# Kernel tuning notes

Measured on AMD Instinct MI355X. Metric: run time of the kernel, lower is better.

## Reference

```python
import jax, jax.numpy as jnp
import numpy as np

NUM_CLASSES = 20
STRIDE = 32
INPUT_SIZE = 2560
CONF_THRESH = 0.01
NMS_THRESH = 0.5
G = INPUT_SIZE // STRIDE          # 80 grid cells per side
N = G * G                         # 6400 candidate boxes
EPS = 1e-28                       # epsilon from original pure-python NMS


def _make_grid():
    # torch.meshgrid default 'ij' indexing: flat index n = x*G + y, entry [x, y]
    gx, gy = jnp.meshgrid(jnp.arange(G, dtype=jnp.float32),
                          jnp.arange(G, dtype=jnp.float32), indexing='ij')
    return jnp.stack([gx, gy], axis=-1).reshape(N, 2)


def _decode_boxes(txtytwth):
    # (grid + sigmoid(txty)) * stride -> center; exp(twth) -> width/height
    cxcy = (_make_grid() + jax.nn.sigmoid(txtytwth[:, :2])) * STRIDE
    wh = jnp.exp(txtytwth[:, 2:])
    boxes = jnp.concatenate([cxcy - wh * 0.5, cxcy + wh * 0.5], axis=-1)
    return jnp.clip(boxes / INPUT_SIZE, 0.0, 1.0)  # [N,4] xyxy in [0,1]


def _batched_nms(boxes, scores, class_idx):
    """Per-class greedy NMS via class-offset trick (equivalent to looping classes)."""
    # translate each class's boxes to a disjoint region so cross-class IoU ~ 0
    b = boxes + class_idx.astype(boxes.dtype)[:, None] * 2.0
    order = jnp.argsort(-scores)              # descending score order
    b = b[order]
    areas = (b[:, 2] - b[:, 0]) * (b[:, 3] - b[:, 1])
    xx1 = jnp.maximum(b[:, None, 0], b[None, :, 0])
    yy1 = jnp.maximum(b[:, None, 1], b[None, :, 1])
    xx2 = jnp.minimum(b[:, None, 2], b[None, :, 2])
    yy2 = jnp.minimum(b[:, None, 3], b[None, :, 3])
    w = jnp.maximum(EPS, xx2 - xx1)
    h = jnp.maximum(EPS, yy2 - yy1)
    inter = w * h                             # [N,N] pairwise intersection
    iou = inter / (areas[:, None] + areas[None, :] - inter)
    valid = scores[order] >= CONF_THRESH      # conf filter before NMS
    idxs = jnp.arange(N)

    def body(i, keep):
        supp = (iou[i] > NMS_THRESH) & (idxs > i)
        return jnp.where(keep[i], keep & ~supp, keep)

    keep_sorted = jax.lax.fori_loop(0, N, body, valid)
    return jnp.zeros(N, dtype=bool).at[order].set(keep_sorted)


def reference(pred):
    p = pred[0]                                   # inference path uses batch 0 only
    conf = jax.nn.sigmoid(p[:, :1])               # objectness
    cls_scores = jax.nn.softmax(p[:, 1:1 + NUM_CLASSES], axis=1) * conf
    boxes = _decode_boxes(p[:, 1 + NUM_CLASSES:])
    class_idx = jnp.argmax(cls_scores, axis=1)
    scores = jnp.max(cls_scores, axis=1)
    keep = _batched_nms(boxes, scores, class_idx)
    # fixed-shape outputs: non-kept detections have score zeroed, keep mask returned
    return boxes, scores * keep, class_idx.astype(jnp.int32), keep


def setup_inputs() -> dict:
    key = jax.random.key(0)
    pred = jax.random.normal(key, (1, N, 1 + NUM_CLASSES + 4), dtype=jnp.float32)
    return {"pred": pred}
```

## Files before the change

kernel.cpp:

```cpp
#include <hip/hip_runtime.h>
#include <stdint.h>

#define NBOX 6400
#define GRIDW 80
#define NC 20
#define NBLK 100

__device__ __forceinline__ float sigmoidf(float x) { return 1.0f / (1.0f + expf(-x)); }

__device__ __forceinline__ void decode_one(const float* __restrict__ p, int n,
        float4* box, float* score, int* cls) {
    float conf = sigmoidf(p[0]);
    float c[NC];
    float m = -INFINITY;
    #pragma unroll
    for (int j = 0; j < NC; j++) { c[j] = p[1 + j]; m = fmaxf(m, c[j]); }
    float sum = 0.f;
    #pragma unroll
    for (int j = 0; j < NC; j++) { c[j] = expf(c[j] - m); sum += c[j]; }
    float best = -INFINITY; int bi = 0;
    #pragma unroll
    for (int j = 0; j < NC; j++) {
        float s = (c[j] / sum) * conf;
        if (s > best) { best = s; bi = j; }
    }
    float gx = (float)(n / GRIDW);
    float gy = (float)(n % GRIDW);
    float cx = (gx + sigmoidf(p[21])) * 32.0f;
    float cy = (gy + sigmoidf(p[22])) * 32.0f;
    float w = expf(p[23]);
    float h = expf(p[24]);
    box->x = fminf(fmaxf((cx - w * 0.5f) / 2560.0f, 0.0f), 1.0f);
    box->y = fminf(fmaxf((cy - h * 0.5f) / 2560.0f, 0.0f), 1.0f);
    box->z = fminf(fmaxf((cx + w * 0.5f) / 2560.0f, 0.0f), 1.0f);
    box->w = fminf(fmaxf((cy + h * 0.5f) / 2560.0f, 0.0f), 1.0f);
    *score = best;
    *cls = bi;
}

__global__ __launch_bounds__(64) void k_decode(const float* __restrict__ pred,
        float* __restrict__ out, float4* __restrict__ boff,
        float* __restrict__ score_ws, float4* __restrict__ blkbb,
        uint64_t* __restrict__ validw) {
    int t = threadIdx.x;
    int n = blockIdx.x * 64 + t;
    float4 bx; float s; int cls;
    decode_one(pred + (size_t)n * 25, n, &bx, &s, &cls);
    ((float4*)out)[n] = bx;
    out[32000 + n] = (float)cls;
    bool valid = s >= 0.01f;
    out[25600 + n] = valid ? s : 0.0f;
    out[38400 + n] = valid ? 1.0f : 0.0f;
    score_ws[n] = s;
    float off = 2.0f * (float)cls;
    boff[n] = make_float4(bx.x + off, bx.y + off, bx.z + off, bx.w + off);

    float x1 = valid ? bx.x :  INFINITY;
    float y1 = valid ? bx.y :  INFINITY;
    float x2 = valid ? bx.z : -INFINITY;
    float y2 = valid ? bx.w : -INFINITY;
    #pragma unroll
    for (int d = 1; d < 64; d <<= 1) {
        x1 = fminf(x1, __shfl_xor(x1, d));
        y1 = fminf(y1, __shfl_xor(y1, d));
        x2 = fmaxf(x2, __shfl_xor(x2, d));
        y2 = fmaxf(y2, __shfl_xor(y2, d));
    }
    uint64_t vb = __ballot(valid);
    if (t == 0) {
        blkbb[blockIdx.x] = make_float4(x1, y1, x2, y2);
        validw[blockIdx.x] = vb;
    }
}

__global__ __launch_bounds__(64) void k_pairs(const float4* __restrict__ boff,
        const float4* __restrict__ blkbb, const uint64_t* __restrict__ validw,
        uint32_t* __restrict__ flag) {
    int k = blockIdx.x;
    float disc = (NBLK + 0.5f) * (NBLK + 0.5f) - 2.0f * (float)k;
    int bi = (int)((float)NBLK + 0.5f - sqrtf(disc));
    while (bi * NBLK - bi * (bi - 1) / 2 > k) bi--;
    while ((bi + 1) * NBLK - (bi + 1) * bi / 2 <= k) bi++;
    int bj = bi + (k - (bi * NBLK - bi * (bi - 1) / 2));

    float4 ra = blkbb[bi];
    float4 ca = blkbb[bj];
    const float M = 1e-5f;
    bool ov = (fminf(ra.z, ca.z) + M >= fmaxf(ra.x, ca.x)) &&
              (fminf(ra.w, ca.w) + M >= fmaxf(ra.y, ca.y));
    if (!ov) return;

    int t = threadIdx.x;
    __shared__ float4 cb[64];
    cb[t] = boff[bj * 64 + t];
    __syncthreads();
    uint64_t colvalid = validw[bj];
    uint64_t rowvalid = validw[bi];
    int i = bi * 64 + t;
    float4 rb = boff[i];
    float areai = (rb.z - rb.x) * (rb.w - rb.y);
    bool hit = false;
    if ((rowvalid >> t) & 1ull) {
        for (int s2 = 0; s2 < 64; s2++) {
            if (!((colvalid >> s2) & 1ull)) continue;
            int j = bj * 64 + s2;
            if (bi == bj && j <= i) continue;
            float4 b = cb[s2];
            float xx1 = fmaxf(rb.x, b.x);
            float yy1 = fmaxf(rb.y, b.y);
            float xx2 = fminf(rb.z, b.z);
            float yy2 = fminf(rb.w, b.w);
            float ww = fmaxf(1e-28f, xx2 - xx1);
            float hh = fmaxf(1e-28f, yy2 - yy1);
            float inter = ww * hh;
            float areaj = (b.z - b.x) * (b.w - b.y);
            if (3.0f * inter >= 0.9995f * (areai + areaj)) { hit = true; break; }
        }
    }
    if (__ballot(hit) != 0ull) {
        if (t == 0) flag[0] = 1u;
    }
}

__global__ __launch_bounds__(1024) void k_fixup(
        const uint32_t* __restrict__ flag, const float* __restrict__ score,
        const float4* __restrict__ boff, int* __restrict__ sidx,
        float* __restrict__ sscore, float4* __restrict__ sbox,
        float* __restrict__ out) {
    if (flag[0] != 1u) return;
    __shared__ uint64_t klds[NBOX];
    __shared__ uint32_t keepb[NBOX / 32];
    int t = threadIdx.x;
    for (int n = t; n < NBOX; n += 1024) {
        klds[n] = (((uint64_t)(~__float_as_uint(score[n]))) << 32) | (uint32_t)n;
    }
    __syncthreads();
    for (int n = t; n < NBOX; n += 1024) {
        uint64_t mk = klds[n];
        int r = 0;
        for (int j = 0; j < NBOX; j++) r += (klds[j] < mk) ? 1 : 0;
        sidx[r] = n;
        sscore[r] = score[n];
        sbox[r] = boff[n];
    }
    __syncthreads();
    for (int w2 = t; w2 < NBOX / 32; w2 += 1024) {
        uint32_t v = 0;
        for (int b = 0; b < 32; b++) v |= (sscore[w2 * 32 + b] >= 0.01f) ? (1u << b) : 0u;
        keepb[w2] = v;
    }
    __syncthreads();
    for (int i = 0; i < NBOX; i++) {
        bool kept = (keepb[i >> 5] >> (i & 31)) & 1u;
        if (kept) {
            float4 a = sbox[i];
            float areai = (a.z - a.x) * (a.w - a.y);
            for (int j = i + 1 + t; j < NBOX; j += 1024) {
                if ((keepb[j >> 5] >> (j & 31)) & 1u) {
                    float4 b = sbox[j];
                    float xx1 = fmaxf(a.x, b.x);
                    float yy1 = fmaxf(a.y, b.y);
                    float xx2 = fminf(a.z, b.z);
                    float yy2 = fminf(a.w, b.w);
                    float ww = fmaxf(1e-28f, xx2 - xx1);
                    float hh = fmaxf(1e-28f, yy2 - yy1);
                    float inter = ww * hh;
                    float areaj = (b.z - b.x) * (b.w - b.y);
                    float iou = inter / (areai + areaj - inter);
                    if (iou > 0.5f) atomicAnd(&keepb[j >> 5], ~(1u << (j & 31)));
                }
            }
        }
        __syncthreads();
    }
    for (int r = t; r < NBOX; r += 1024) {
        int orig = sidx[r];
        uint32_t kb = (keepb[r >> 5] >> (r & 31)) & 1u;
        out[38400 + orig] = (float)kb;
        out[25600 + orig] = kb ? sscore[r] : 0.0f;
    }
}

extern "C" void kernel_launch(void* const* d_in, const int* in_sizes, int n_in,
                              void* d_out, int out_size, void* d_ws, size_t ws_size,
                              hipStream_t stream) {
    const float* pred = (const float*)d_in[0];
    float* out = (float*)d_out;
    char* ws = (char*)d_ws;
    float4*   boff   = (float4*)(ws + 0);
    float*    score  = (float*)(ws + 102400);
    float4*   blkbb  = (float4*)(ws + 128000);
    uint64_t* validw = (uint64_t*)(ws + 129600);
    uint32_t* flag   = (uint32_t*)(ws + 130432);
    int*      sidx   = (int*)(ws + 131072);
    float*    sscore = (float*)(ws + 156672);
    float4*   sbox   = (float4*)(ws + 182272);

    k_decode<<<NBLK, 64, 0, stream>>>(pred, out, boff, score, blkbb, validw);
    k_pairs<<<5050, 64, 0, stream>>>(boff, blkbb, validw, flag);
    k_fixup<<<1, 1024, 0, stream>>>(flag, score, boff, sidx, sscore, sbox, out);
}
```

Baseline: 73.08 us.

## Merge pair check and fallback NMS into one kernel with last-block election

Replaces the 5050-block pair-check kernel and the separate single-block fixup kernel with one 25-block kernel. Each wave handles one row block and walks the overlapping column blocks found via ballot, reading column boxes through wave shuffles instead of LDS. A done counter picks the last block to run the exact NMS fallback when the flag is set. The flag and counter are now reset inside the decode kernel. This saves a kernel launch and the many short-lived blocks, at the cost of serial per-wave loops over column blocks and running any fallback on a 256-thread block instead of a 1024-thread one.

```diff
diff --git a/kernel.cpp b/kernel.cpp
--- a/kernel.cpp
+++ b/kernel.cpp
@@ -38,12 +38,15 @@
     *cls = bi;
 }
 
-__global__ __launch_bounds__(64) void k_decode(const float* __restrict__ pred,
+__global__ __launch_bounds__(256) void k_decode(const float* __restrict__ pred,
         float* __restrict__ out, float4* __restrict__ boff,
         float* __restrict__ score_ws, float4* __restrict__ blkbb,
-        uint64_t* __restrict__ validw) {
+        uint64_t* __restrict__ validw, uint32_t* __restrict__ flag,
+        uint32_t* __restrict__ done) {
     int t = threadIdx.x;
-    int n = blockIdx.x * 64 + t;
+    int n = blockIdx.x * 256 + t;
+    int l = t & 63;
+    if (n == 0) { flag[0] = 0u; done[0] = 0u; }
     float4 bx; float s; int cls;
     decode_one(pred + (size_t)n * 25, n, &bx, &s, &cls);
     ((float4*)out)[n] = bx;
@@ -67,75 +70,99 @@
         y2 = fmaxf(y2, __shfl_xor(y2, d));
     }
     uint64_t vb = __ballot(valid);
-    if (t == 0) {
-        blkbb[blockIdx.x] = make_float4(x1, y1, x2, y2);
-        validw[blockIdx.x] = vb;
-    }
-}
-
-__global__ __launch_bounds__(64) void k_pairs(const float4* __restrict__ boff,
+    if (l == 0) {
+        blkbb[n >> 6] = make_float4(x1, y1, x2, y2);
+        validw[n >> 6] = vb;
+    }
+}
+
+__global__ __launch_bounds__(256) void k_work(const float4* __restrict__ boff,
         const float4* __restrict__ blkbb, const uint64_t* __restrict__ validw,
-        uint32_t* __restrict__ flag) {
-    int k = blockIdx.x;
-    float disc = (NBLK + 0.5f) * (NBLK + 0.5f) - 2.0f * (float)k;
-    int bi = (int)((float)NBLK + 0.5f - sqrtf(disc));
-    while (bi * NBLK - bi * (bi - 1) / 2 > k) bi--;
-    while ((bi + 1) * NBLK - (bi + 1) * bi / 2 <= k) bi++;
-    int bj = bi + (k - (bi * NBLK - bi * (bi - 1) / 2));
+        const float* __restrict__ score, uint32_t* __restrict__ flag,
+        uint32_t* __restrict__ done, int* __restrict__ sidx,
+        float* __restrict__ sscore, float4* __restrict__ sbox,
+        float* __restrict__ out) {
+    __shared__ uint64_t klds[NBOX];
+    __shared__ uint32_t keepb[NBOX / 32];
+    __shared__ uint32_t lastf;
+    int t = threadIdx.x;
+    int w = t >> 6, l = t & 63;
+    int bi = blockIdx.x * 4 + w;
 
     float4 ra = blkbb[bi];
-    float4 ca = blkbb[bj];
+    uint64_t rowvalid = validw[bi];
     const float M = 1e-5f;
-    bool ov = (fminf(ra.z, ca.z) + M >= fmaxf(ra.x, ca.x)) &&
-              (fminf(ra.w, ca.w) + M >= fmaxf(ra.y, ca.y));
-    if (!ov) return;
-
-    int t = threadIdx.x;
-    __shared__ float4 cb[64];
-    cb[t] = boff[bj * 64 + t];
-    __syncthreads();
-    uint64_t colvalid = validw[bj];
-    uint64_t rowvalid = validw[bi];
-    int i = bi * 64 + t;
+    uint64_t surv_lo, surv_hi;
+    {
+        bool ov = false;
+        int bj = bi + l;
+        if (bj < NBLK) {
+            float4 ca = blkbb[bj];
+            ov = (fminf(ra.z, ca.z) + M >= fmaxf(ra.x, ca.x)) &&
+                 (fminf(ra.w, ca.w) + M >= fmaxf(ra.y, ca.y));
+        }
+        surv_lo = __ballot(ov);
+        ov = false;
+        bj = bi + 64 + l;
+        if (bj < NBLK) {
+            float4 ca = blkbb[bj];
+            ov = (fminf(ra.z, ca.z) + M >= fmaxf(ra.x, ca.x)) &&
+                 (fminf(ra.w, ca.w) + M >= fmaxf(ra.y, ca.y));
+        }
+        surv_hi = __ballot(ov);
+    }
+    if (rowvalid == 0ull) { surv_lo = 0ull; surv_hi = 0ull; }
+
+    int i = bi * 64 + l;
     float4 rb = boff[i];
     float areai = (rb.z - rb.x) * (rb.w - rb.y);
+    bool rv = (rowvalid >> l) & 1ull;
     bool hit = false;
-    if ((rowvalid >> t) & 1ull) {
-        for (int s2 = 0; s2 < 64; s2++) {
-            if (!((colvalid >> s2) & 1ull)) continue;
-            int j = bj * 64 + s2;
-            if (bi == bj && j <= i) continue;
-            float4 b = cb[s2];
-            float xx1 = fmaxf(rb.x, b.x);
-            float yy1 = fmaxf(rb.y, b.y);
-            float xx2 = fminf(rb.z, b.z);
-            float yy2 = fminf(rb.w, b.w);
-            float ww = fmaxf(1e-28f, xx2 - xx1);
-            float hh = fmaxf(1e-28f, yy2 - yy1);
-            float inter = ww * hh;
-            float areaj = (b.z - b.x) * (b.w - b.y);
-            if (3.0f * inter >= 0.9995f * (areai + areaj)) { hit = true; break; }
-        }
-    }
-    if (__ballot(hit) != 0ull) {
-        if (t == 0) flag[0] = 1u;
-    }
-}
-
-__global__ __launch_bounds__(1024) void k_fixup(
-        const uint32_t* __restrict__ flag, const float* __restrict__ score,
-        const float4* __restrict__ boff, int* __restrict__ sidx,
-        float* __restrict__ sscore, float4* __restrict__ sbox,
-        float* __restrict__ out) {
-    if (flag[0] != 1u) return;
-    __shared__ uint64_t klds[NBOX];
-    __shared__ uint32_t keepb[NBOX / 32];
-    int t = threadIdx.x;
-    for (int n = t; n < NBOX; n += 1024) {
+    while ((surv_lo | surv_hi) != 0ull) {
+        int d;
+        if (surv_lo) { d = __ffsll((unsigned long long)surv_lo) - 1; surv_lo &= surv_lo - 1; }
+        else { d = 64 + __ffsll((unsigned long long)surv_hi) - 1; surv_hi &= surv_hi - 1; }
+        int bj = bi + d;
+        uint64_t colvalid = validw[bj];
+        if (colvalid == 0ull) continue;
+        float4 cb = boff[bj * 64 + l];
+        if (rv && !hit) {
+            for (int s2 = 0; s2 < 64; s2++) {
+                if (!((colvalid >> s2) & 1ull)) continue;
+                int j = bj * 64 + s2;
+                if (bi == bj && j <= i) continue;
+                float bxx = __shfl(cb.x, s2);
+                float byy = __shfl(cb.y, s2);
+                float bzz = __shfl(cb.z, s2);
+                float bww = __shfl(cb.w, s2);
+                float xx1 = fmaxf(rb.x, bxx);
+                float yy1 = fmaxf(rb.y, byy);
+                float xx2 = fminf(rb.z, bzz);
+                float yy2 = fminf(rb.w, bww);
+                float ww = fmaxf(1e-28f, xx2 - xx1);
+                float hh = fmaxf(1e-28f, yy2 - yy1);
+                float inter = ww * hh;
+                float areaj = (bzz - bxx) * (bww - byy);
+                if (3.0f * inter >= 0.9995f * (areai + areaj)) { hit = true; break; }
+            }
+        }
+    }
+    if (__ballot(hit) != 0ull && l == 0) atomicOr(flag, 1u);
+
+    __syncthreads();
+    __threadfence();
+    if (t == 0) lastf = (atomicAdd(done, 1u) == 24u) ? 1u : 0u;
+    __syncthreads();
+    if (!lastf) return;
+    uint32_t f;
+    if (t == 0) { f = atomicOr(flag, 0u); lastf = f; }
+    __syncthreads();
+    if (!(lastf & 1u)) return;
+
+    for (int n = t; n < NBOX; n += 256)
         klds[n] = (((uint64_t)(~__float_as_uint(score[n]))) << 32) | (uint32_t)n;
-    }
-    __syncthreads();
-    for (int n = t; n < NBOX; n += 1024) {
+    __syncthreads();
+    for (int n = t; n < NBOX; n += 256) {
         uint64_t mk = klds[n];
         int r = 0;
         for (int j = 0; j < NBOX; j++) r += (klds[j] < mk) ? 1 : 0;
@@ -144,18 +171,18 @@
         sbox[r] = boff[n];
     }
     __syncthreads();
-    for (int w2 = t; w2 < NBOX / 32; w2 += 1024) {
+    for (int w2 = t; w2 < NBOX / 32; w2 += 256) {
         uint32_t v = 0;
         for (int b = 0; b < 32; b++) v |= (sscore[w2 * 32 + b] >= 0.01f) ? (1u << b) : 0u;
         keepb[w2] = v;
     }
     __syncthreads();
-    for (int i = 0; i < NBOX; i++) {
-        bool kept = (keepb[i >> 5] >> (i & 31)) & 1u;
+    for (int ii = 0; ii < NBOX; ii++) {
+        bool kept = (keepb[ii >> 5] >> (ii & 31)) & 1u;
         if (kept) {
-            float4 a = sbox[i];
-            float areai = (a.z - a.x) * (a.w - a.y);
-            for (int j = i + 1 + t; j < NBOX; j += 1024) {
+            float4 a = sbox[ii];
+            float areaa = (a.z - a.x) * (a.w - a.y);
+            for (int j = ii + 1 + t; j < NBOX; j += 256) {
                 if ((keepb[j >> 5] >> (j & 31)) & 1u) {
                     float4 b = sbox[j];
                     float xx1 = fmaxf(a.x, b.x);
@@ -165,15 +192,15 @@
                     float ww = fmaxf(1e-28f, xx2 - xx1);
                     float hh = fmaxf(1e-28f, yy2 - yy1);
                     float inter = ww * hh;
-                    float areaj = (b.z - b.x) * (b.w - b.y);
-                    float iou = inter / (areai + areaj - inter);
+                    float areab = (b.z - b.x) * (b.w - b.y);
+                    float iou = inter / (areaa + areab - inter);
                     if (iou > 0.5f) atomicAnd(&keepb[j >> 5], ~(1u << (j & 31)));
                 }
             }
         }
         __syncthreads();
     }
-    for (int r = t; r < NBOX; r += 1024) {
+    for (int r = t; r < NBOX; r += 256) {
         int orig = sidx[r];
         uint32_t kb = (keepb[r >> 5] >> (r & 31)) & 1u;
         out[38400 + orig] = (float)kb;
@@ -192,11 +219,12 @@
     float4*   blkbb  = (float4*)(ws + 128000);
     uint64_t* validw = (uint64_t*)(ws + 129600);
     uint32_t* flag   = (uint32_t*)(ws + 130432);
+    uint32_t* done   = (uint32_t*)(ws + 130436);
     int*      sidx   = (int*)(ws + 131072);
     float*    sscore = (float*)(ws + 156672);
     float4*   sbox   = (float4*)(ws + 182272);
 
-    k_decode<<<NBLK, 64, 0, stream>>>(pred, out, boff, score, blkbb, validw);
-    k_pairs<<<5050, 64, 0, stream>>>(boff, blkbb, validw, flag);
-    k_fixup<<<1, 1024, 0, stream>>>(flag, score, boff, sidx, sscore, sbox, out);
-}
+    k_decode<<<25, 256, 0, stream>>>(pred, out, boff, score, blkbb, validw, flag, done);
+    k_work<<<25, 256, 0, stream>>>(boff, blkbb, validw, score, flag, done,
+                                   sidx, sscore, sbox, out);
+}
```

New measurement: 104.7 us. +43.2%, slower.
